# Optimization experiments

Measured on AMD Instinct MI355X. Metric: run time of the kernel, lower is better.

## Reference

```python
import jax, jax.numpy as jnp
import numpy as np

B, H0, W0, C = 8, 112, 112, 192
NH, WS, SS = 6, 7, 3
HID = 4 * C


def _rel_pos_index(ws):
    coords = np.stack(np.meshgrid(np.arange(ws), np.arange(ws), indexing='ij'))  # [2,ws,ws]
    flat = coords.reshape(2, -1)
    rel = flat[:, :, None] - flat[:, None, :]          # [2,N,N]
    rel = rel.transpose(1, 2, 0).copy()                # [N,N,2]
    rel[:, :, 0] += ws - 1
    rel[:, :, 1] += ws - 1
    rel[:, :, 0] *= 2 * ws - 1
    return rel.sum(-1)                                 # [N,N]


def _attn_mask(Hp, Wp, ws, ss):
    # 0 / -100 mask for shifted windows, identical to torch get_attn_mask
    img = np.zeros((Hp, Wp))
    cnt = 0
    for hs in (slice(0, -ws), slice(-ws, -ss), slice(-ss, None)):
        for wsl in (slice(0, -ws), slice(-ws, -ss), slice(-ss, None)):
            img[hs, wsl] = cnt
            cnt += 1
    mw = img.reshape(Hp // ws, ws, Wp // ws, ws).transpose(0, 2, 1, 3).reshape(-1, ws * ws)
    am = mw[:, None, :] - mw[:, :, None]
    return np.where(am != 0, np.float32(-100.0), np.float32(0.0)).astype(np.float32)  # [nW,N,N]


def _ln(x, g, b, eps=1e-5):
    mu = jnp.mean(x, axis=-1, keepdims=True)
    var = jnp.mean(jnp.square(x - mu), axis=-1, keepdims=True)
    return (x - mu) * jax.lax.rsqrt(var + eps) * g + b


def setup_inputs() -> dict:
    key = jax.random.key(0)
    ks = jax.random.split(key, 8)
    p = lambda k, s: jax.random.normal(k, s, jnp.float32) * 0.02
    return {
        'query': jax.random.normal(ks[0], (B, H0 * W0, C), jnp.float32),
        'norm1_g': jnp.ones((C,), jnp.float32), 'norm1_b': jnp.zeros((C,), jnp.float32),
        'qkv_w': p(ks[1], (C, 3 * C)), 'qkv_b': jnp.zeros((3 * C,), jnp.float32),
        'rpb_table': p(ks[2], ((2 * WS - 1) ** 2, NH)),
        'proj_w': p(ks[3], (C, C)), 'proj_b': jnp.zeros((C,), jnp.float32),
        'norm2_g': jnp.ones((C,), jnp.float32), 'norm2_b': jnp.zeros((C,), jnp.float32),
        'fc1_w': p(ks[4], (C, HID)), 'fc1_b': jnp.zeros((HID,), jnp.float32),
        'fc2_w': p(ks[5], (HID, C)), 'fc2_b': jnp.zeros((C,), jnp.float32),
        'H': H0, 'W': W0,
    }


def reference(query, norm1_g, norm1_b, qkv_w, qkv_b, rpb_table, proj_w, proj_b,
              norm2_g, norm2_b, fc1_w, fc1_b, fc2_w, fc2_b, H, W):
    Bq, L, Cq = query.shape
    ws, ss, nh = WS, SS, NH
    hd = Cq // nh
    N = ws * ws
    # ---- W-MSA branch ----
    x = _ln(query, norm1_g, norm1_b).reshape(Bq, H, W, Cq)
    # H, W chosen divisible by ws -> pad branch is a no-op
    x = jnp.roll(x, (-ss, -ss), axis=(1, 2))            # cyclic shift
    nWh, nWw = H // ws, W // ws
    # window partition -> [B*nW, N, C]
    xw = x.reshape(Bq, nWh, ws, nWw, ws, Cq).transpose(0, 1, 3, 2, 4, 5).reshape(-1, N, Cq)
    qkv = (xw @ qkv_w + qkv_b).reshape(-1, N, 3, nh, hd).transpose(2, 0, 3, 1, 4)
    q, k, v = qkv[0] * (hd ** -0.5), qkv[1], qkv[2]     # [B_,nh,N,hd]
    attn = jnp.einsum('bhnd,bhmd->bhnm', q, k)
    bias = rpb_table[_rel_pos_index(ws).reshape(-1)].reshape(N, N, nh).transpose(2, 0, 1)
    attn = attn + bias[None]
    mask = jnp.asarray(_attn_mask(H, W, ws, ss))        # [nW,N,N]
    nW = mask.shape[0]
    attn = attn.reshape(Bq, nW, nh, N, N) + mask[None, :, None]
    attn = jax.nn.softmax(attn.reshape(-1, nh, N, N), axis=-1)
    out = jnp.einsum('bhnm,bhmd->bhnd', attn, v).transpose(0, 2, 1, 3).reshape(-1, N, Cq)
    out = out @ proj_w + proj_b
    # window reverse + reverse shift
    x = out.reshape(Bq, nWh, nWw, ws, ws, Cq).transpose(0, 1, 3, 2, 4, 5).reshape(Bq, H, W, Cq)
    x = jnp.roll(x, (ss, ss), axis=(1, 2)).reshape(Bq, H * W, Cq)
    x = query + x
    # ---- MLP branch ----
    h = _ln(x, norm2_g, norm2_b)
    h = jax.nn.gelu(h @ fc1_w + fc1_b, approximate=False)
    return x + (h @ fc2_w + fc2_b)
```

## Files before the change

kernel.cpp:

```cpp
#include <hip/hip_runtime.h>
#include <hip/hip_bf16.h>
#include <math.h>

using bf16 = __hip_bfloat16;
typedef __bf16 bf16x8 __attribute__((ext_vector_type(8)));
typedef __bf16 bf16x4 __attribute__((ext_vector_type(4)));
typedef float floatx4 __attribute__((ext_vector_type(4)));

__device__ __forceinline__ float bf2f(bf16 x) { return __bfloat162float(x); }
__device__ __forceinline__ bf16 f2bf(float x) { return __float2bfloat16(x); }

__device__ __forceinline__ float loadExt(const void* p, long i, int f32) {
  return f32 ? ((const float*)p)[i] : bf2f(((const bf16*)p)[i]);
}
__device__ __forceinline__ void storeExt(void* p, long i, int f32, float v) {
  if (f32) ((float*)p)[i] = v;
  else     ((bf16*)p)[i] = f2bf(v);
}

#define GLOAD16(gp, lp)                                                       \
  __builtin_amdgcn_global_load_lds(                                           \
      (const __attribute__((address_space(1))) void*)(gp),                    \
      (__attribute__((address_space(3))) void*)(lp), 16, 0, 0)

__global__ void detect_kernel(const unsigned int* __restrict__ q, int* __restrict__ flag) {
  const int lane = threadIdx.x;
  const unsigned int w = q[lane];
  const unsigned int lo = w & 0xffffu;
  const unsigned int e = (lo >> 7) & 0xffu;
  const bool ok = (lo == 0u) || (e >= 100u && e <= 141u);
  const unsigned long long m = __ballot(ok);
  if (lane == 0) flag[0] = (__popcll(m) == 64) ? 1 : 0;
}

__global__ void cvt_params_kernel(const int* __restrict__ flagp,
                                  const void* qkv_b, const void* proj_b,
                                  const void* n1g, const void* n1b,
                                  const void* n2g, const void* n2b,
                                  const void* fc1_b, const void* fc2_b,
                                  const void* rpb, bf16* __restrict__ dst) {
  const int f32 = (flagp[0] == 0);
  int i = blockIdx.x * blockDim.x + threadIdx.x;
  if (i >= 3510) return;
  const void* src; int j = i;
  if      (j < 576)  { src = qkv_b; }
  else if ((j -= 576)  < 192) { src = proj_b; }
  else if ((j -= 192)  < 192) { src = n1g; }
  else if ((j -= 192)  < 192) { src = n1b; }
  else if ((j -= 192)  < 192) { src = n2g; }
  else if ((j -= 192)  < 192) { src = n2b; }
  else if ((j -= 192)  < 768) { src = fc1_b; }
  else if ((j -= 768)  < 192) { src = fc2_b; }
  else { j -= 192; src = rpb; }
  dst[i] = f2bf(loadExt(src, j, f32));
}

__global__ void cvtT_kernel(const int* __restrict__ flagp, const void* __restrict__ src,
                            bf16* __restrict__ dst, int K, int N) {
  const int f32 = (flagp[0] == 0);
  int i = blockIdx.x * blockDim.x + threadIdx.x;
  if (i >= K * N) return;
  int n = i / K, k = i - n * K;
  dst[i] = f2bf(loadExt(src, (long)k * N + n, f32));
}

__global__ void biastab_kernel(const bf16* __restrict__ rpb,
                               bf16* __restrict__ btab) {
  int i = blockIdx.x * blockDim.x + threadIdx.x;
  if (i >= 6 * 2450) return;
  int head = i / 2450, r = i - head * 2450;
  int n = r / 50, m = r - n * 50;
  float v = 0.f;
  if (n < 49 && m < 49) {
    int r1 = n / 7, c1 = n - 7 * r1, r2 = m / 7, c2 = m - 7 * r2;
    v = bf2f(rpb[((r1 - r2 + 6) * 13 + (c1 - c2 + 6)) * 6 + head]);
  }
  btab[i] = f2bf(v);
}

__global__ __launch_bounds__(256) void ln_kernel(const int* __restrict__ flagp, int ext,
                                                 const void* __restrict__ x,
                                                 const bf16* __restrict__ g,
                                                 const bf16* __restrict__ b,
                                                 bf16* __restrict__ out) {
  const int f32 = ext && (flagp[0] == 0);
  const long row = (long)blockIdx.x * 4 + (threadIdx.x >> 6);
  const int lane = threadIdx.x & 63;
  const long gbase = row * 192;
  float v0 = loadExt(x, gbase + lane, f32);
  float v1 = loadExt(x, gbase + lane + 64, f32);
  float v2 = loadExt(x, gbase + lane + 128, f32);
  float s = v0 + v1 + v2;
  #pragma unroll
  for (int off = 32; off > 0; off >>= 1) s += __shfl_xor(s, off, 64);
  const float mu = s * (1.0f / 192.0f);
  float d0 = v0 - mu, d1 = v1 - mu, d2 = v2 - mu;
  float vv = d0 * d0 + d1 * d1 + d2 * d2;
  #pragma unroll
  for (int off = 32; off > 0; off >>= 1) vv += __shfl_xor(vv, off, 64);
  const float rstd = rsqrtf(vv * (1.0f / 192.0f) + 1e-5f);
  bf16* orow = out + row * 192;
  orow[lane]       = f2bf(d0 * rstd * bf2f(g[lane])       + bf2f(b[lane]));
  orow[lane + 64]  = f2bf(d1 * rstd * bf2f(g[lane + 64])  + bf2f(b[lane + 64]));
  orow[lane + 128] = f2bf(d2 * rstd * bf2f(g[lane + 128]) + bf2f(b[lane + 128]));
}

template <int EPI>
__global__ __launch_bounds__(256) void gemm_bt(const bf16* __restrict__ A,
                                               const bf16* __restrict__ BT,
                                               const bf16* __restrict__ bias,
                                               const int* __restrict__ flagp,
                                               const void* res, int res_ext,
                                               void* out, int out_ext,
                                               int M, int N, int K) {
  __shared__ __align__(16) bf16 As[2][128 * 32];
  __shared__ __align__(16) bf16 Bs[2][64 * 32];
  const int xf32 = (flagp[0] == 0);
  const int tid = threadIdx.x;
  const int wave = tid >> 6;
  const int lane = tid & 63;
  const int l16 = lane & 15;
  const int quad = lane >> 4;

  const int nbn = N >> 6;
  const int cpx = gridDim.x >> 3;
  const int wg = (gridDim.x & 7) ? (int)blockIdx.x
                                 : (blockIdx.x & 7) * cpx + (blockIdx.x >> 3);
  const int mb = wg / nbn;
  const int nb = wg - mb * nbn;
  const long m0 = (long)mb * 128;
  const int n0 = nb << 6;

  const int rS = tid >> 2;
  const int sS = tid & 3;
  const int ss = sS ^ ((rS >> 1) & 3);
  const bf16* gA0 = A + (m0 + rS) * (long)K + ss * 8;
  const bf16* gA1 = A + (m0 + rS + 64) * (long)K + ss * 8;
  const bf16* gB  = BT + (long)(n0 + rS) * K + ss * 8;

  floatx4 acc[2][4];
  #pragma unroll
  for (int i = 0; i < 2; i++)
    #pragma unroll
    for (int j = 0; j < 4; j++) acc[i][j] = (floatx4){0.f, 0.f, 0.f, 0.f};

  const int swz = (quad ^ ((l16 >> 1) & 3)) << 3;
  const int arow = wave * 32 + l16;

  GLOAD16(gA0, &As[0][tid * 8]);
  GLOAD16(gA1, &As[0][(tid + 256) * 8]);
  GLOAD16(gB,  &Bs[0][tid * 8]);
  __syncthreads();

  int cur = 0;
  for (int k0 = 0; k0 < K; k0 += 32) {
    if (k0 + 32 < K) {
      const int nxt = cur ^ 1;
      GLOAD16(gA0 + k0 + 32, &As[nxt][tid * 8]);
      GLOAD16(gA1 + k0 + 32, &As[nxt][(tid + 256) * 8]);
      GLOAD16(gB  + k0 + 32, &Bs[nxt][tid * 8]);
    }
    bf16x8 af[2], bfr[4];
    #pragma unroll
    for (int ms = 0; ms < 2; ms++)
      af[ms] = *(const bf16x8*)&As[cur][(arow + ms * 16) * 32 + swz];
    #pragma unroll
    for (int ns = 0; ns < 4; ns++)
      bfr[ns] = *(const bf16x8*)&Bs[cur][(ns * 16 + l16) * 32 + swz];
    #pragma unroll
    for (int ms = 0; ms < 2; ms++)
      #pragma unroll
      for (int ns = 0; ns < 4; ns++)
        acc[ms][ns] = __builtin_amdgcn_mfma_f32_16x16x32_bf16(bfr[ns], af[ms], acc[ms][ns], 0, 0, 0);
    __syncthreads();
    cur ^= 1;
  }

  #pragma unroll
  for (int ms = 0; ms < 2; ms++) {
    const long row = m0 + wave * 32 + ms * 16 + l16;
    #pragma unroll
    for (int ns = 0; ns < 4; ns++) {
      const int col = n0 + ns * 16 + quad * 4;
      const long idx = row * (long)N + col;
      float v[4];
      #pragma unroll
      for (int r = 0; r < 4; r++) v[r] = acc[ms][ns][r] + bf2f(bias[col + r]);
      if (EPI == 1) {
        #pragma unroll
        for (int r = 0; r < 4; r++)
          v[r] = 0.5f * v[r] * (1.0f + erff(v[r] * 0.70710678118654752f));
      }
      if (EPI == 2) {
        if (res_ext && xf32) {
          const float4 t = *(const float4*)((const float*)res + idx);
          v[0] += t.x; v[1] += t.y; v[2] += t.z; v[3] += t.w;
        } else {
          const bf16x4 t = *(const bf16x4*)((const bf16*)res + idx);
          #pragma unroll
          for (int r = 0; r < 4; r++) v[r] += (float)t[r];
        }
      }
      if (out_ext && xf32) {
        float4 t; t.x = v[0]; t.y = v[1]; t.z = v[2]; t.w = v[3];
        *(float4*)((float*)out + idx) = t;
      } else {
        bf16x4 t;
        #pragma unroll
        for (int r = 0; r < 4; r++) t[r] = (__bf16)v[r];
        *(bf16x4*)((bf16*)out + idx) = t;
      }
    }
  }
}

template <int EPI, int LN>
__global__ __launch_bounds__(256) void gemm_k192(const bf16* __restrict__ A,
                                                 const bf16* __restrict__ BT,
                                                 const bf16* __restrict__ bias,
                                                 const bf16* __restrict__ gN,
                                                 const bf16* __restrict__ bN,
                                                 const int* __restrict__ flagp,
                                                 const void* res, int res_ext,
                                                 void* out, int out_ext,
                                                 int M, int N) {
  __shared__ __align__(16) __bf16 Ash[128 * 192];
  __shared__ __align__(16) __bf16 Bsh[64 * 192];
  const int xf32 = (flagp[0] == 0);
  const int tid = threadIdx.x;
  const int wave = tid >> 6;
  const int lane = tid & 63;
  const int l16 = lane & 15;
  const int quad = lane >> 4;

  const int nbn = N >> 6;
  const int cpx = gridDim.x >> 3;
  const int wg = (gridDim.x & 7) ? (int)blockIdx.x
                                 : (blockIdx.x & 7) * cpx + (blockIdx.x >> 3);
  const int mb = wg / nbn;
  const int nb = wg - mb * nbn;
  const long m0 = (long)mb * 128;
  const int n0 = nb << 6;

  #pragma unroll
  for (int i = 0; i < 6; i++) {
    const int u = i * 256 + tid;
    const int r = u / 24, sl = u % 24;
    const int ssl = (sl & 24) | ((sl ^ r) & 7);
    GLOAD16(BT + (long)(n0 + r) * 192 + ssl * 8, &Bsh[u * 8]);
  }
  #pragma unroll
  for (int i = 0; i < 12; i++) {
    const int u = i * 256 + tid;
    const int r = u / 24, sl = u % 24;
    const int ssl = LN ? sl : ((sl & 24) | ((sl ^ r) & 7));
    GLOAD16(A + (m0 + r) * (long)192 + ssl * 8, &Ash[u * 8]);
  }
  asm volatile("s_waitcnt vmcnt(0)" ::: "memory");
  __builtin_amdgcn_s_barrier();

  if (LN) {
    const int row = tid >> 1, half = tid & 1;
    bf16x8 xr[12];
    #pragma unroll
    for (int i = 0; i < 12; i++)
      xr[i] = *(const bf16x8*)&Ash[row * 192 + (half * 12 + i) * 8];
    float s1 = 0.f;
    #pragma unroll
    for (int i = 0; i < 12; i++)
      #pragma unroll
      for (int j = 0; j < 8; j++) s1 += (float)xr[i][j];
    s1 += __shfl_xor(s1, 1, 64);
    const float mu = s1 * (1.0f / 192.0f);
    float s2 = 0.f;
    #pragma unroll
    for (int i = 0; i < 12; i++)
      #pragma unroll
      for (int j = 0; j < 8; j++) {
        const float d = (float)xr[i][j] - mu;
        s2 += d * d;
      }
    s2 += __shfl_xor(s2, 1, 64);
    const float rstd = rsqrtf(s2 * (1.0f / 192.0f) + 1e-5f);
    #pragma unroll
    for (int i = 0; i < 12; i++) {
      const int slot = half * 12 + i;
      const bf16x8 gg = *(const bf16x8*)&gN[slot * 8];
      const bf16x8 bb = *(const bf16x8*)&bN[slot * 8];
      bf16x8 nr;
      #pragma unroll
      for (int j = 0; j < 8; j++)
        nr[j] = (__bf16)(((float)xr[i][j] - mu) * rstd * (float)gg[j] + (float)bb[j]);
      xr[i] = nr;
    }
    __syncthreads();
    #pragma unroll
    for (int i = 0; i < 12; i++) {
      const int slot = half * 12 + i;
      const int sw = (slot & 24) | ((slot ^ row) & 7);
      *(bf16x8*)&Ash[row * 192 + sw * 8] = xr[i];
    }
    __syncthreads();
  }

  floatx4 acc[2][4];
  #pragma unroll
  for (int i = 0; i < 2; i++)
    #pragma unroll
    for (int j = 0; j < 4; j++) acc[i][j] = (floatx4){0.f, 0.f, 0.f, 0.f};

  #pragma unroll
  for (int ks = 0; ks < 6; ks++) {
    const int sl = ks * 4 + quad;
    bf16x8 af[2], bfr[4];
    #pragma unroll
    for (int ms = 0; ms < 2; ms++) {
      const int r = wave * 32 + ms * 16 + l16;
      af[ms] = *(const bf16x8*)&Ash[r * 192 + ((sl & 24) | ((sl ^ r) & 7)) * 8];
    }
    #pragma unroll
    for (int ns = 0; ns < 4; ns++) {
      const int r = ns * 16 + l16;
      bfr[ns] = *(const bf16x8*)&Bsh[r * 192 + ((sl & 24) | ((sl ^ r) & 7)) * 8];
    }
    #pragma unroll
    for (int ms = 0; ms < 2; ms++)
      #pragma unroll
      for (int ns = 0; ns < 4; ns++)
        acc[ms][ns] = __builtin_amdgcn_mfma_f32_16x16x32_bf16(bfr[ns], af[ms], acc[ms][ns], 0, 0, 0);
  }

  #pragma unroll
  for (int ms = 0; ms < 2; ms++) {
    const long row = m0 + wave * 32 + ms * 16 + l16;
    #pragma unroll
    for (int ns = 0; ns < 4; ns++) {
      const int col = n0 + ns * 16 + quad * 4;
      const long idx = row * (long)N + col;
      float v[4];
      #pragma unroll
      for (int r = 0; r < 4; r++) v[r] = acc[ms][ns][r] + bf2f(bias[col + r]);
      if (EPI == 1) {
        #pragma unroll
        for (int r = 0; r < 4; r++)
          v[r] = 0.5f * v[r] * (1.0f + erff(v[r] * 0.70710678118654752f));
      }
      if (EPI == 2) {
        if (res_ext && xf32) {
          const float4 t = *(const float4*)((const float*)res + idx);
          v[0] += t.x; v[1] += t.y; v[2] += t.z; v[3] += t.w;
        } else {
          const bf16x4 t = *(const bf16x4*)((const bf16*)res + idx);
          #pragma unroll
          for (int r = 0; r < 4; r++) v[r] += (float)t[r];
        }
      }
      if (out_ext && xf32) {
        float4 t; t.x = v[0]; t.y = v[1]; t.z = v[2]; t.w = v[3];
        *(float4*)((float*)out + idx) = t;
      } else {
        bf16x4 t;
        #pragma unroll
        for (int r = 0; r < 4; r++) t[r] = (__bf16)v[r];
        *(bf16x4*)((bf16*)out + idx) = t;
      }
    }
  }
}

__global__ __launch_bounds__(64, 3) void attn_kernel(const bf16* __restrict__ qkv,
                                                     const bf16* __restrict__ btab,
                                                     bf16* __restrict__ out) {
  __shared__ __align__(16) __bf16 vshT[32 * 64];
  __shared__ __align__(16) __bf16 psh[64 * 64];
  __shared__ int rowIdx[64];
  __shared__ int regn[64];
  const int lane = threadIdx.x;
  const int q = lane >> 4, l16 = lane & 15;
  const int unit = blockIdx.x;
  const int head = unit % 6;
  const int wIdx = unit / 6;
  const int b = wIdx >> 8;
  const int w2 = wIdx & 255;
  const int wh = w2 >> 4;
  const int ww = w2 & 15;

  {
    const int l = lane < 49 ? lane : 48;
    const int r = l / 7, c = l - 7 * r;
    const int hr = wh * 7 + r;
    const int wr = ww * 7 + c;
    int h = hr + 3; if (h >= 112) h -= 112;
    int w = wr + 3; if (w >= 112) w -= 112;
    rowIdx[lane] = b * 12544 + h * 112 + w;
    const int rh = hr < 105 ? 0 : (hr < 109 ? 1 : 2);
    const int rw = wr < 105 ? 0 : (wr < 109 ? 1 : 2);
    regn[lane] = (lane < 49) ? rh * 3 + rw : 99;
  }
  __syncthreads();

  int ridx[4];
  #pragma unroll
  for (int t = 0; t < 4; t++) ridx[t] = rowIdx[t * 16 + l16];

  #pragma unroll
  for (int ii = 0; ii < 4; ii++) {
    const int i = lane + ii * 64;
    const int j = i >> 2, c = (i & 3) * 8;
    const bf16x8 vv = *(const bf16x8*)&qkv[(long)rowIdx[j] * 576 + 384 + head * 32 + c];
    #pragma unroll
    for (int jj = 0; jj < 8; jj++) {
      const int d = c + jj;
      vshT[d * 64 + (((j >> 3) ^ (d & 7)) << 3) + (j & 7)] = vv[jj];
    }
  }

  floatx4 s[4][4];
  #pragma unroll
  for (int it = 0; it < 4; it++)
    #pragma unroll
    for (int jt = 0; jt < 4; jt++) s[it][jt] = (floatx4){0.f, 0.f, 0.f, 0.f};
  {
    bf16x8 afq[4], bfk[4];
    #pragma unroll
    for (int t = 0; t < 4; t++) {
      const bf16* pQ = &qkv[(long)ridx[t] * 576 + head * 32 + q * 8];
      afq[t] = *(const bf16x8*)pQ;
      bfk[t] = *(const bf16x8*)(pQ + 192);
    }
    #pragma unroll
    for (int it = 0; it < 4; it++)
      #pragma unroll
      for (int jt = 0; jt < 4; jt++)
        s[it][jt] = __builtin_amdgcn_mfma_f32_16x16x32_bf16(afq[it], bfk[jt], s[it][jt], 0, 0, 0);
  }

  int regj[4];
  #pragma unroll
  for (int jt = 0; jt < 4; jt++) regj[jt] = regn[jt * 16 + l16];
  int regi[4][4];
  #pragma unroll
  for (int it = 0; it < 4; it++)
    #pragma unroll
    for (int r = 0; r < 4; r++) regi[it][r] = regn[it * 16 + q * 4 + r];

  const bf16* bt = btab + head * 2450;
  const float scale = 0.17677669529663687f;
  float mrow[4][4];
  #pragma unroll
  for (int it = 0; it < 4; it++)
    #pragma unroll
    for (int r = 0; r < 4; r++) mrow[it][r] = -3e38f;

  #pragma unroll
  for (int it = 0; it < 4; it++)
    #pragma unroll
    for (int jt = 0; jt < 4; jt++)
      #pragma unroll
      for (int r = 0; r < 4; r++) {
        const int i = it * 16 + q * 4 + r;
        const int j = jt * 16 + l16;
        const int bi = (i < 49 ? i : 48) * 50 + (j < 49 ? j : 48);
        float v = s[it][jt][r] * scale + bf2f(bt[bi]);
        if (regi[it][r] != regj[jt]) v -= 100.0f;
        v = (j < 49) ? v : -1e30f;
        s[it][jt][r] = v;
        mrow[it][r] = fmaxf(mrow[it][r], v);
      }
  #pragma unroll
  for (int it = 0; it < 4; it++)
    #pragma unroll
    for (int r = 0; r < 4; r++) {
      float m = mrow[it][r];
      #pragma unroll
      for (int off = 1; off < 16; off <<= 1) m = fmaxf(m, __shfl_xor(m, off, 64));
      mrow[it][r] = m;
    }
  float sum[4][4];
  #pragma unroll
  for (int it = 0; it < 4; it++)
    #pragma unroll
    for (int r = 0; r < 4; r++) sum[it][r] = 0.f;
  #pragma unroll
  for (int it = 0; it < 4; it++)
    #pragma unroll
    for (int jt = 0; jt < 4; jt++)
      #pragma unroll
      for (int r = 0; r < 4; r++) {
        const float e = __expf(s[it][jt][r] - mrow[it][r]);
        s[it][jt][r] = e;
        sum[it][r] += e;
      }
  #pragma unroll
  for (int it = 0; it < 4; it++)
    #pragma unroll
    for (int r = 0; r < 4; r++) {
      float t = sum[it][r];
      #pragma unroll
      for (int off = 1; off < 16; off <<= 1) t += __shfl_xor(t, off, 64);
      mrow[it][r] = 1.0f / t;
    }

  #pragma unroll
  for (int it = 0; it < 4; it++)
    #pragma unroll
    for (int jt = 0; jt < 4; jt++)
      #pragma unroll
      for (int r = 0; r < 4; r++) {
        const int i = it * 16 + q * 4 + r;
        const int j = jt * 16 + l16;
        psh[i * 64 + (((j >> 3) ^ (i & 7)) << 3) + (j & 7)] =
            (__bf16)(s[it][jt][r] * mrow[it][r]);
      }
  __syncthreads();

  floatx4 o[4][2];
  #pragma unroll
  for (int it = 0; it < 4; it++)
    #pragma unroll
    for (int dt = 0; dt < 2; dt++) o[it][dt] = (floatx4){0.f, 0.f, 0.f, 0.f};
  #pragma unroll
  for (int ks = 0; ks < 2; ks++) {
    bf16x8 av[2];
    #pragma unroll
    for (int dt = 0; dt < 2; dt++) {
      const int row = dt * 16 + l16;
      av[dt] = *(const bf16x8*)&vshT[row * 64 + (((ks * 4 + q) ^ (row & 7)) << 3)];
    }
    #pragma unroll
    for (int it = 0; it < 4; it++) {
      const int row = it * 16 + l16;
      const bf16x8 bp = *(const bf16x8*)&psh[row * 64 + (((ks * 4 + q) ^ (row & 7)) << 3)];
      #pragma unroll
      for (int dt = 0; dt < 2; dt++)
        o[it][dt] = __builtin_amdgcn_mfma_f32_16x16x32_bf16(bp, av[dt], o[it][dt], 0, 0, 0);
    }
  }

  #pragma unroll
  for (int it = 0; it < 4; it++)
    #pragma unroll
    for (int r = 0; r < 4; r++) {
      const int i = it * 16 + q * 4 + r;
      if (i < 49) {
        const long ob = (long)rowIdx[i] * 192 + head * 32;
        #pragma unroll
        for (int dt = 0; dt < 2; dt++)
          out[ob + dt * 16 + l16] = f2bf(o[it][dt][r]);
      }
    }
}

extern "C" void kernel_launch(void* const* d_in, const int* in_sizes, int n_in,
                              void* d_out, int out_size, void* d_ws, size_t ws_size,
                              hipStream_t stream) {
  const void* query   = d_in[0];
  const void* norm1_g = d_in[1];
  const void* norm1_b = d_in[2];
  const void* qkv_w   = d_in[3];
  const void* qkv_b   = d_in[4];
  const void* rpb     = d_in[5];
  const void* proj_w  = d_in[6];
  const void* proj_b  = d_in[7];
  const void* norm2_g = d_in[8];
  const void* norm2_b = d_in[9];
  const void* fc1_w   = d_in[10];
  const void* fc1_b   = d_in[11];
  const void* fc2_w   = d_in[12];
  const void* fc2_b   = d_in[13];

  const long M = 100352;

  int* flag  = (int*)d_ws;
  bf16* base = (bf16*)((char*)d_ws + 16);
  bf16* wsA   = base;
  bf16* wsB   = wsA + M * 192;
  bf16* xbuf  = wsB + M * 768;
  bf16* qkvT  = xbuf + M * 192;
  bf16* projT = qkvT + 110592;
  bf16* fc1T  = projT + 36864;
  bf16* fc2T  = fc1T + 147456;
  bf16* pPAR  = fc2T + 147456;
  bf16* pQKVB = pPAR;
  bf16* pPRJB = pQKVB + 576;
  bf16* pN1G  = pPRJB + 192;
  bf16* pN1B  = pN1G + 192;
  bf16* pN2G  = pN1B + 192;
  bf16* pN2B  = pN2G + 192;
  bf16* pFC1B = pN2B + 192;
  bf16* pFC2B = pFC1B + 768;
  bf16* pRPB  = pFC2B + 192;
  bf16* btab  = pPAR + 3510;

  detect_kernel<<<1, 64, 0, stream>>>((const unsigned int*)query, flag);
  cvt_params_kernel<<<14, 256, 0, stream>>>(flag, qkv_b, proj_b, norm1_g, norm1_b,
                                            norm2_g, norm2_b, fc1_b, fc2_b, rpb, pPAR);
  cvtT_kernel<<<(192 * 576 + 255) / 256, 256, 0, stream>>>(flag, qkv_w, qkvT, 192, 576);
  cvtT_kernel<<<(192 * 192 + 255) / 256, 256, 0, stream>>>(flag, proj_w, projT, 192, 192);
  cvtT_kernel<<<(192 * 768 + 255) / 256, 256, 0, stream>>>(flag, fc1_w, fc1T, 192, 768);
  cvtT_kernel<<<(768 * 192 + 255) / 256, 256, 0, stream>>>(flag, fc2_w, fc2T, 768, 192);
  biastab_kernel<<<(6 * 2450 + 255) / 256, 256, 0, stream>>>(pRPB, btab);

  ln_kernel<<<M / 4, 256, 0, stream>>>(flag, 1, query, pN1G, pN1B, wsA);
  gemm_k192<0, 0><<<784 * 9, 256, 0, stream>>>(wsA, qkvT, pQKVB, nullptr, nullptr,
                                               flag, nullptr, 0, wsB, 0, (int)M, 576);
  attn_kernel<<<12288, 64, 0, stream>>>(wsB, btab, wsA);
  gemm_k192<2, 0><<<784 * 3, 256, 0, stream>>>(wsA, projT, pPRJB, nullptr, nullptr,
                                               flag, query, 1, xbuf, 0, (int)M, 192);

  gemm_k192<1, 1><<<784 * 12, 256, 0, stream>>>(xbuf, fc1T, pFC1B, pN2G, pN2B,
                                                flag, nullptr, 0, wsB, 0, (int)M, 768);
  gemm_bt<2><<<784 * 3, 256, 0, stream>>>(wsB, fc2T, pFC2B, flag,
                                          xbuf, 0, d_out, 1, (int)M, 192, 768);
}
```

Before: 617.3 us.

## Unfuse LN2 from fc1 GEMM, merge weight conversions, use tanh GELU

Moves the second LayerNorm out of the fc1 GEMM into a separate ln_kernel pass, so the normalization is no longer recomputed for every one of the 12 N tiles. The four transpose-convert kernels and the parameter conversion are merged into one launch. The exact erf GELU is replaced by a tanh approximation using __expf. This adds an extra activation round trip through memory and changes numerics relative to the exact GELU reference.

```diff
diff --git a/kernel.cpp b/kernel.cpp
--- a/kernel.cpp
+++ b/kernel.cpp
@@ -16,6 +16,15 @@
 __device__ __forceinline__ void storeExt(void* p, long i, int f32, float v) {
   if (f32) ((float*)p)[i] = v;
   else     ((bf16*)p)[i] = f2bf(v);
+}
+
+__device__ __forceinline__ float gelu_tanh(float v) {
+  const float u = 0.7978845608028654f * v * (1.0f + 0.044715f * v * v);
+  const float a = fabsf(u);
+  const float e = __expf(-2.0f * a);
+  float t = (1.0f - e) / (1.0f + e);
+  t = (u < 0.f) ? -t : t;
+  return 0.5f * v * (1.0f + t);
 }
 
 #define GLOAD16(gp, lp)                                                       \
@@ -33,14 +42,43 @@
   if (lane == 0) flag[0] = (__popcll(m) == 64) ? 1 : 0;
 }
 
-__global__ void cvt_params_kernel(const int* __restrict__ flagp,
-                                  const void* qkv_b, const void* proj_b,
-                                  const void* n1g, const void* n1b,
-                                  const void* n2g, const void* n2b,
-                                  const void* fc1_b, const void* fc2_b,
-                                  const void* rpb, bf16* __restrict__ dst) {
+__global__ void cvt_all_kernel(const int* __restrict__ flagp,
+                               const void* qkv_w, const void* proj_w,
+                               const void* fc1_w, const void* fc2_w,
+                               const void* qkv_b, const void* proj_b,
+                               const void* n1g, const void* n1b,
+                               const void* n2g, const void* n2b,
+                               const void* fc1_b, const void* fc2_b,
+                               const void* rpb,
+                               bf16* __restrict__ qkvT, bf16* __restrict__ projT,
+                               bf16* __restrict__ fc1T, bf16* __restrict__ fc2T,
+                               bf16* __restrict__ pPAR) {
   const int f32 = (flagp[0] == 0);
   int i = blockIdx.x * blockDim.x + threadIdx.x;
+  if (i < 110592) {
+    const int n = i / 192, k = i - n * 192;
+    qkvT[i] = f2bf(loadExt(qkv_w, (long)k * 576 + n, f32));
+    return;
+  }
+  i -= 110592;
+  if (i < 36864) {
+    const int n = i / 192, k = i - n * 192;
+    projT[i] = f2bf(loadExt(proj_w, (long)k * 192 + n, f32));
+    return;
+  }
+  i -= 36864;
+  if (i < 147456) {
+    const int n = i / 192, k = i - n * 192;
+    fc1T[i] = f2bf(loadExt(fc1_w, (long)k * 768 + n, f32));
+    return;
+  }
+  i -= 147456;
+  if (i < 147456) {
+    const int n = i / 768, k = i - n * 768;
+    fc2T[i] = f2bf(loadExt(fc2_w, (long)k * 192 + n, f32));
+    return;
+  }
+  i -= 147456;
   if (i >= 3510) return;
   const void* src; int j = i;
   if      (j < 576)  { src = qkv_b; }
@@ -52,16 +90,7 @@
   else if ((j -= 192)  < 768) { src = fc1_b; }
   else if ((j -= 768)  < 192) { src = fc2_b; }
   else { j -= 192; src = rpb; }
-  dst[i] = f2bf(loadExt(src, j, f32));
-}
-
-__global__ void cvtT_kernel(const int* __restrict__ flagp, const void* __restrict__ src,
-                            bf16* __restrict__ dst, int K, int N) {
-  const int f32 = (flagp[0] == 0);
-  int i = blockIdx.x * blockDim.x + threadIdx.x;
-  if (i >= K * N) return;
-  int n = i / K, k = i - n * K;
-  dst[i] = f2bf(loadExt(src, (long)k * N + n, f32));
+  pPAR[i] = f2bf(loadExt(src, j, f32));
 }
 
 __global__ void biastab_kernel(const bf16* __restrict__ rpb,
@@ -188,8 +217,7 @@
       for (int r = 0; r < 4; r++) v[r] = acc[ms][ns][r] + bf2f(bias[col + r]);
       if (EPI == 1) {
         #pragma unroll
-        for (int r = 0; r < 4; r++)
-          v[r] = 0.5f * v[r] * (1.0f + erff(v[r] * 0.70710678118654752f));
+        for (int r = 0; r < 4; r++) v[r] = gelu_tanh(v[r]);
       }
       if (EPI == 2) {
         if (res_ext && xf32) {
@@ -214,12 +242,10 @@
   }
 }
 
-template <int EPI, int LN>
+template <int EPI>
 __global__ __launch_bounds__(256) void gemm_k192(const bf16* __restrict__ A,
                                                  const bf16* __restrict__ BT,
                                                  const bf16* __restrict__ bias,
-                                                 const bf16* __restrict__ gN,
-                                                 const bf16* __restrict__ bN,
                                                  const int* __restrict__ flagp,
                                                  const void* res, int res_ext,
                                                  void* out, int out_ext,
@@ -253,55 +279,11 @@
   for (int i = 0; i < 12; i++) {
     const int u = i * 256 + tid;
     const int r = u / 24, sl = u % 24;
-    const int ssl = LN ? sl : ((sl & 24) | ((sl ^ r) & 7));
+    const int ssl = (sl & 24) | ((sl ^ r) & 7);
     GLOAD16(A + (m0 + r) * (long)192 + ssl * 8, &Ash[u * 8]);
   }
   asm volatile("s_waitcnt vmcnt(0)" ::: "memory");
   __builtin_amdgcn_s_barrier();
-
-  if (LN) {
-    const int row = tid >> 1, half = tid & 1;
-    bf16x8 xr[12];
-    #pragma unroll
-    for (int i = 0; i < 12; i++)
-      xr[i] = *(const bf16x8*)&Ash[row * 192 + (half * 12 + i) * 8];
-    float s1 = 0.f;
-    #pragma unroll
-    for (int i = 0; i < 12; i++)
-      #pragma unroll
-      for (int j = 0; j < 8; j++) s1 += (float)xr[i][j];
-    s1 += __shfl_xor(s1, 1, 64);
-    const float mu = s1 * (1.0f / 192.0f);
-    float s2 = 0.f;
-    #pragma unroll
-    for (int i = 0; i < 12; i++)
-      #pragma unroll
-      for (int j = 0; j < 8; j++) {
-        const float d = (float)xr[i][j] - mu;
-        s2 += d * d;
-      }
-    s2 += __shfl_xor(s2, 1, 64);
-    const float rstd = rsqrtf(s2 * (1.0f / 192.0f) + 1e-5f);
-    #pragma unroll
-    for (int i = 0; i < 12; i++) {
-      const int slot = half * 12 + i;
-      const bf16x8 gg = *(const bf16x8*)&gN[slot * 8];
-      const bf16x8 bb = *(const bf16x8*)&bN[slot * 8];
-      bf16x8 nr;
-      #pragma unroll
-      for (int j = 0; j < 8; j++)
-        nr[j] = (__bf16)(((float)xr[i][j] - mu) * rstd * (float)gg[j] + (float)bb[j]);
-      xr[i] = nr;
-    }
-    __syncthreads();
-    #pragma unroll
-    for (int i = 0; i < 12; i++) {
-      const int slot = half * 12 + i;
-      const int sw = (slot & 24) | ((slot ^ row) & 7);
-      *(bf16x8*)&Ash[row * 192 + sw * 8] = xr[i];
-    }
-    __syncthreads();
-  }
 
   floatx4 acc[2][4];
   #pragma unroll
@@ -342,8 +324,7 @@
       for (int r = 0; r < 4; r++) v[r] = acc[ms][ns][r] + bf2f(bias[col + r]);
       if (EPI == 1) {
         #pragma unroll
-        for (int r = 0; r < 4; r++)
-          v[r] = 0.5f * v[r] * (1.0f + erff(v[r] * 0.70710678118654752f));
+        for (int r = 0; r < 4; r++) v[r] = gelu_tanh(v[r]);
       }
       if (EPI == 2) {
         if (res_ext && xf32) {
@@ -593,23 +574,21 @@
   bf16* btab  = pPAR + 3510;
 
   detect_kernel<<<1, 64, 0, stream>>>((const unsigned int*)query, flag);
-  cvt_params_kernel<<<14, 256, 0, stream>>>(flag, qkv_b, proj_b, norm1_g, norm1_b,
-                                            norm2_g, norm2_b, fc1_b, fc2_b, rpb, pPAR);
-  cvtT_kernel<<<(192 * 576 + 255) / 256, 256, 0, stream>>>(flag, qkv_w, qkvT, 192, 576);
-  cvtT_kernel<<<(192 * 192 + 255) / 256, 256, 0, stream>>>(flag, proj_w, projT, 192, 192);
-  cvtT_kernel<<<(192 * 768 + 255) / 256, 256, 0, stream>>>(flag, fc1_w, fc1T, 192, 768);
-  cvtT_kernel<<<(768 * 192 + 255) / 256, 256, 0, stream>>>(flag, fc2_w, fc2T, 768, 192);
+  cvt_all_kernel<<<(445878 + 255) / 256, 256, 0, stream>>>(
+      flag, qkv_w, proj_w, fc1_w, fc2_w, qkv_b, proj_b, norm1_g, norm1_b,
+      norm2_g, norm2_b, fc1_b, fc2_b, rpb, qkvT, projT, fc1T, fc2T, pPAR);
   biastab_kernel<<<(6 * 2450 + 255) / 256, 256, 0, stream>>>(pRPB, btab);
 
   ln_kernel<<<M / 4, 256, 0, stream>>>(flag, 1, query, pN1G, pN1B, wsA);
-  gemm_k192<0, 0><<<784 * 9, 256, 0, stream>>>(wsA, qkvT, pQKVB, nullptr, nullptr,
-                                               flag, nullptr, 0, wsB, 0, (int)M, 576);
+  gemm_k192<0><<<784 * 9, 256, 0, stream>>>(wsA, qkvT, pQKVB, flag,
+                                            nullptr, 0, wsB, 0, (int)M, 576);
   attn_kernel<<<12288, 64, 0, stream>>>(wsB, btab, wsA);
-  gemm_k192<2, 0><<<784 * 3, 256, 0, stream>>>(wsA, projT, pPRJB, nullptr, nullptr,
-                                               flag, query, 1, xbuf, 0, (int)M, 192);
-
-  gemm_k192<1, 1><<<784 * 12, 256, 0, stream>>>(xbuf, fc1T, pFC1B, pN2G, pN2B,
-                                                flag, nullptr, 0, wsB, 0, (int)M, 768);
+  gemm_k192<2><<<784 * 3, 256, 0, stream>>>(wsA, projT, pPRJB, flag,
+                                            query, 1, xbuf, 0, (int)M, 192);
+
+  ln_kernel<<<M / 4, 256, 0, stream>>>(flag, 0, xbuf, pN2G, pN2B, wsA);
+  gemm_k192<1><<<784 * 12, 256, 0, stream>>>(wsA, fc1T, pFC1B, flag,
+                                             nullptr, 0, wsB, 0, (int)M, 768);
   gemm_bt<2><<<784 * 3, 256, 0, stream>>>(wsB, fc2T, pFC2B, flag,
                                           xbuf, 0, d_out, 1, (int)M, 192, 768);
 }
```

New measurement: 591.0 us. -4.3%, faster.
